# Optimization experiments

Hardware: AMD Instinct MI355X
Metric: run time of the kernel (lower is better)

The kernel has to match this reference:

```python
import jax, jax.numpy as jnp
import numpy as np

B, T = 8, 2048
IN, OUT = 1024, 1024
M, C = 32, 32
MIN_P, MAX_P = 1.0, 1024.0
EPS = 1e-5


def setup_inputs() -> dict:
    key = jax.random.key(0)
    ks = jax.random.split(key, 4)
    x = jax.random.normal(ks[0], (B, T, IN), dtype=jnp.float32)
    # pre: Linear(IN, 2*M + 2*OUT); mix: Linear(2*M*C, OUT)
    pre_w = jax.random.normal(ks[1], (IN, 2 * M + 2 * OUT), dtype=jnp.float32) / np.sqrt(IN)
    pre_b = jnp.zeros((2 * M + 2 * OUT,), jnp.float32)
    mix_w = jax.random.normal(ks[2], (2 * M * C, OUT), dtype=jnp.float32) / np.sqrt(2 * M * C)
    mix_b = jnp.zeros((OUT,), jnp.float32)
    # FFA decay/oscillation params (paper init): gamma_{m,c} = exp(-|a_m| + i b_c)
    a = jnp.linspace(1e-6, 0.5, M, dtype=jnp.float32)
    b = 2.0 * jnp.pi / jnp.linspace(MIN_P, MAX_P, C, dtype=jnp.float32)
    return dict(x=x, pre_w=pre_w, pre_b=pre_b, mix_w=mix_w, mix_b=mix_b, a=a, b=b)


def _ffa(u, a, b):
    """Complex-decay linear recurrence: s_t = gamma * s_{t-1} + u_t (s_0 = 0).

    u: [B,T,M] real input (broadcast over context dim C).
    Returns all states: [B,T,M,C] complex64.
    """
    log_gamma = (-jnp.abs(a))[:, None] + 1j * b[None, :]  # [M,C]
    gamma = jnp.exp(log_gamma).astype(jnp.complex64)
    Tn = u.shape[1]
    h = jnp.broadcast_to(u[..., None].astype(jnp.complex64), u.shape + (C,))  # [B,T,M,C]
    h = jnp.moveaxis(h, 1, 0)  # [T,B,M,C]
    p = jnp.broadcast_to(gamma, (Tn, 1, M, C))  # [T,1,M,C] time-invariant decay

    def combine(e1, e2):
        p1, h1 = e1
        p2, h2 = e2
        return (p1 * p2, h1 * p2 + h2)

    _, hs = jax.lax.associative_scan(combine, (p, h), axis=0)
    return jnp.moveaxis(hs, 0, 1)  # [B,T,M,C]


def reference(x, pre_w, pre_b, mix_w, mix_b, a, b):
    Bx, Tx, _ = x.shape
    pre = x @ pre_w + pre_b  # [B,T,2M+2OUT]
    y, thru, gate = jnp.split(pre, [M, M + OUT], axis=-1)
    gate = jax.nn.sigmoid(gate)
    in_gate, out_gate = gate[..., :M], gate[..., M:]
    s = _ffa(y * in_gate, a, b)  # [B,T,M,C] complex64
    # torch.view_as_real -> [...,M,C,2] then flatten -> interleaved (re,im)
    zr = jnp.stack([s.real, s.imag], axis=-1).reshape(Bx, Tx, 2 * M * C)
    z = zr @ mix_w + mix_b  # [B,T,OUT]
    # LayerNorm (no affine)
    z = (z - z.mean(-1, keepdims=True)) / jnp.sqrt(z.var(-1, keepdims=True) + EPS)
    out = z * out_gate + thru * (1.0 - out_gate)
    return out, s
```

## Files before the change

kernel.cpp:

```cpp
#include <hip/hip_runtime.h>
#include <stdint.h>

typedef __attribute__((ext_vector_type(2))) __bf16 bf16x2;
typedef __attribute__((ext_vector_type(4))) __bf16 bf16x4;
typedef __attribute__((ext_vector_type(8))) __bf16 bf16x8;
typedef __attribute__((ext_vector_type(4))) float f32x4;

#define DEV __device__ __forceinline__

DEV void g2lds16(const void* g, void* l) {
  __builtin_amdgcn_global_load_lds(
      (const __attribute__((address_space(1))) void*)g,
      (__attribute__((address_space(3))) void*)l, 16, 0, 0);
}

DEV void barrier_ws() {
  __builtin_amdgcn_sched_barrier(0);
  asm volatile("" ::: "memory");
  __builtin_amdgcn_s_barrier();
  asm volatile("" ::: "memory");
  __builtin_amdgcn_sched_barrier(0);
}

__global__ __launch_bounds__(256) void cvt_f32_bf16(const float* __restrict__ s,
                                                    __bf16* __restrict__ d, int n) {
  int i = (blockIdx.x * 256 + threadIdx.x) * 4;
  if (i >= n) return;
  float4 v = *reinterpret_cast<const float4*>(s + i);
  bf16x4 o;
  o[0] = (__bf16)v.x; o[1] = (__bf16)v.y; o[2] = (__bf16)v.z; o[3] = (__bf16)v.w;
  *reinterpret_cast<bf16x4*>(d + i) = o;
}

__global__ __launch_bounds__(256) void transpose_to_bf16(const float* __restrict__ src,
                                                         __bf16* __restrict__ dst,
                                                         int K, int N, int Npad) {
  __shared__ float tile[32][33];
  int n0 = blockIdx.x * 32, k0 = blockIdx.y * 32;
  int tx = threadIdx.x & 31, ty = threadIdx.x >> 5;
#pragma unroll
  for (int j = 0; j < 4; ++j) {
    int k = k0 + ty + j * 8;
    int n = n0 + tx;
    float v = 0.f;
    if (n < N) v = src[(long)k * N + n];
    tile[ty + j * 8][tx] = v;
  }
  __syncthreads();
#pragma unroll
  for (int j = 0; j < 4; ++j) {
    int n = n0 + ty + j * 8;
    int k = k0 + tx;
    if (n < Npad) dst[(long)n * K + k] = (__bf16)tile[tx][ty + j * 8];
  }
}

#define STAGE_A(d, kh, kc)                                           \
  { g2lds16(A + aoffg0 + (kc), &As[d][(kh)*8192 + q0 * 8]);          \
    g2lds16(A + aoffg1 + (kc), &As[d][(kh)*8192 + q1 * 8]); }
#define STAGE_B(d, kh, kc)                                           \
  { g2lds16(Wt + boffg0 + (kc), &Bs[d][(kh)*8192 + q0 * 8]);         \
    g2lds16(Wt + boffg1 + (kc), &Bs[d][(kh)*8192 + q1 * 8]); }

#define PHASE(d, MQ, KH, READB, STAGE_STMT, TAILWAIT)                         \
  {                                                                           \
    bf16x8 af[4];                                                             \
    _Pragma("unroll") for (int i = 0; i < 4; ++i)                             \
        af[i] = *reinterpret_cast<const bf16x8*>(                             \
            &As[d][(KH)*8192 + aoffl[(MQ)*4 + i]]);                           \
    if (READB) {                                                              \
      _Pragma("unroll") for (int n = 0; n < 4; ++n)                           \
          bw[n] = *reinterpret_cast<const bf16x8*>(                           \
              &Bs[d][(KH)*8192 + boffl[n]]);                                  \
    }                                                                         \
    STAGE_STMT;                                                               \
    barrier_ws();                                                             \
    __builtin_amdgcn_s_setprio(1);                                            \
    _Pragma("unroll") for (int i = 0; i < 4; ++i)                             \
      _Pragma("unroll") for (int n = 0; n < 4; ++n)                           \
          acc[(MQ)*4 + i][n] = __builtin_amdgcn_mfma_f32_16x16x32_bf16(       \
              af[i], bw[n], acc[(MQ)*4 + i][n], 0, 0, 0);                     \
    __builtin_amdgcn_s_setprio(0);                                            \
    TAILWAIT;                                                                 \
    barrier_ws();                                                             \
  }

template <bool OUT_BF16>
__global__ __launch_bounds__(512, 2) void gemm_8p(const __bf16* __restrict__ A,
                                                  const __bf16* __restrict__ Wt,
                                                  const float* __restrict__ bias,
                                                  void* __restrict__ Cout,
                                                  int K, int Nreal, int ldc,
                                                  int gx) {
  __shared__ __bf16 As[2][16384];
  __shared__ __bf16 Bs[2][16384];
  const int tid = threadIdx.x;
  const int lane = tid & 63, wid = tid >> 6;
  const int wr = wid >> 2, wc = wid & 3;

  const int nwg = gridDim.x;
  const int orig = blockIdx.x;
  const int wg = ((orig & 7) * (nwg >> 3)) + (orig >> 3);
  const int tm = (wg / gx) * 256, tn = (wg % gx) * 256;

  f32x4 acc[8][4] = {};
  bf16x8 bw[4];

  const int q0 = tid, q1 = tid + 512;
  const int row0 = ((q0 >> 3) << 1) | ((q0 >> 2) & 1);
  const int c0e = (((q0 & 3) - (q0 >> 3)) & 3) * 8;
  const int row1 = ((q1 >> 3) << 1) | ((q1 >> 2) & 1);
  const int c1e = (((q1 & 3) - (q1 >> 3)) & 3) * 8;
  const long aoffg0 = (long)(tm + row0) * K + c0e;
  const long aoffg1 = (long)(tm + row1) * K + c1e;
  const long boffg0 = (long)(tn + row0) * K + c0e;
  const long boffg1 = (long)(tn + row1) * K + c1e;

  const int l15 = lane & 15, cl = lane >> 4;
  int aoffl[8], boffl[4];
#pragma unroll
  for (int mf = 0; mf < 8; ++mf) {
    int row = wr * 128 + (mf >> 2) * 64 + (mf & 3) * 16 + l15;
    aoffl[mf] = (row >> 1) * 64 + (((row & 1) << 2) | ((cl + (row >> 1)) & 3)) * 8;
  }
#pragma unroll
  for (int nf = 0; nf < 4; ++nf) {
    int row = wc * 64 + nf * 16 + l15;
    boffl[nf] = (row >> 1) * 64 + (((row & 1) << 2) | ((cl + (row >> 1)) & 3)) * 8;
  }

  STAGE_A(0, 0, 0);
  STAGE_B(0, 0, 0);
  STAGE_A(0, 1, 32);
  STAGE_B(0, 1, 32);
  asm volatile("s_waitcnt vmcnt(4)" ::: "memory");
  barrier_ws();

  const int nt = K >> 6;
  for (int T = 0; T < nt - 1; ++T) {
    const int d = T & 1, e = d ^ 1;
    const int kc = (T + 1) << 6;
    PHASE(d, 0, 0, 1, STAGE_A(e, 0, kc), ((void)0));
    PHASE(d, 1, 0, 0, STAGE_B(e, 0, kc),
          asm volatile("s_waitcnt vmcnt(4)" ::: "memory"));
    PHASE(d, 0, 1, 1, STAGE_A(e, 1, kc + 32), ((void)0));
    PHASE(d, 1, 1, 0, STAGE_B(e, 1, kc + 32),
          asm volatile("s_waitcnt vmcnt(4)" ::: "memory"));
  }
  {
    const int d = (nt - 1) & 1;
    PHASE(d, 0, 0, 1, ((void)0), ((void)0));
    PHASE(d, 1, 0, 0, ((void)0),
          asm volatile("s_waitcnt vmcnt(0)" ::: "memory"));
    PHASE(d, 0, 1, 1, ((void)0), ((void)0));
    PHASE(d, 1, 1, 0, ((void)0), ((void)0));
  }

#pragma unroll
  for (int mf = 0; mf < 8; ++mf) {
    const int rg = tm + wr * 128 + (mf >> 2) * 64 + (mf & 3) * 16 + (lane >> 4) * 4;
#pragma unroll
    for (int nf = 0; nf < 4; ++nf) {
      int col = tn + wc * 64 + nf * 16 + l15;
      if (col < Nreal) {
        float bv = bias[col];
#pragma unroll
        for (int r = 0; r < 4; ++r) {
          long row = rg + r;
          float v = acc[mf][nf][r] + bv;
          if (OUT_BF16) ((__bf16*)Cout)[row * (long)ldc + col] = (__bf16)v;
          else          ((float*)Cout)[row * (long)ldc + col] = v;
        }
      }
    }
  }
}

__global__ __launch_bounds__(256) void u_kernel(const __bf16* __restrict__ pre,
                                                float* __restrict__ u) {
  int i = blockIdx.x * 8 + (threadIdx.x >> 5);
  int m = threadIdx.x & 31;
  const __bf16* pr = pre + (long)i * 2112;
  float y = (float)pr[m];
  float g = (float)pr[1056 + m];
  float sg = 1.f / (1.f + expf(-g));
  int b = i >> 11, t = i & 2047;
  u[(long)((b * 32) + m) * 2048 + t] = y * sg;
}

__global__ __launch_bounds__(64) void scan_kernel(const float* __restrict__ u,
                                                  const float* __restrict__ a,
                                                  const float* __restrict__ bfr,
                                                  __bf16* __restrict__ s_bf,
                                                  float* __restrict__ s_re) {
  int blk = blockIdx.x;
  int b = blk >> 4, mp = blk & 15;
  int lane = threadIdx.x;
  int mh = lane >> 5, c = lane & 31;
  int m = mp * 2 + mh;
  const float* ub = u + (long)(b * 32 + m) * 2048;
  float decay = expf(-fabsf(a[m]));
  float gr = decay * cosf(bfr[c]);
  float gi = decay * sinf(bfr[c]);
  float sr = 0.f, si = 0.f;
  long base = (long)b * 2048 * 1024 + m * 32 + c;
  for (int t = 0; t < 2048; ++t) {
    float uv = ub[t];
    float nr = fmaf(gr, sr, fmaf(-gi, si, uv));
    float ni_ = fmaf(gr, si, gi * sr);
    sr = nr; si = ni_;
    long ci = base + (long)t * 1024;
    bf16x2 zv; zv[0] = (__bf16)sr; zv[1] = (__bf16)si;
    *reinterpret_cast<bf16x2*>(s_bf + 2 * ci) = zv;
    s_re[ci] = sr;
  }
}

__global__ __launch_bounds__(256) void ln_gate_kernel(float* __restrict__ z,
                                                      const __bf16* __restrict__ pre) {
  __shared__ float rs[4], rss[4];
  long row = blockIdx.x;
  float* zp = z + row * 1024;
  int tid = threadIdx.x;
  float4 v = *reinterpret_cast<const float4*>(zp + tid * 4);
  float s = v.x + v.y + v.z + v.w;
  float ss = v.x * v.x + v.y * v.y + v.z * v.z + v.w * v.w;
#pragma unroll
  for (int o = 32; o > 0; o >>= 1) {
    s += __shfl_down(s, o, 64);
    ss += __shfl_down(ss, o, 64);
  }
  if ((tid & 63) == 0) { rs[tid >> 6] = s; rss[tid >> 6] = ss; }
  __syncthreads();
  s = rs[0] + rs[1] + rs[2] + rs[3];
  ss = rss[0] + rss[1] + rss[2] + rss[3];
  float mean = s * (1.f / 1024.f);
  float var = ss * (1.f / 1024.f) - mean * mean;
  float rstd = rsqrtf(var + 1e-5f);
  const __bf16* pr = pre + row * 2112;
  bf16x4 th = *reinterpret_cast<const bf16x4*>(pr + 32 + tid * 4);
  bf16x4 og = *reinterpret_cast<const bf16x4*>(pr + 1088 + tid * 4);
  float4 o; float g;
  g = 1.f / (1.f + expf(-(float)og[0])); o.x = (v.x - mean) * rstd * g + (float)th[0] * (1.f - g);
  g = 1.f / (1.f + expf(-(float)og[1])); o.y = (v.y - mean) * rstd * g + (float)th[1] * (1.f - g);
  g = 1.f / (1.f + expf(-(float)og[2])); o.z = (v.z - mean) * rstd * g + (float)th[2] * (1.f - g);
  g = 1.f / (1.f + expf(-(float)og[3])); o.w = (v.w - mean) * rstd * g + (float)th[3] * (1.f - g);
  *reinterpret_cast<float4*>(zp + tid * 4) = o;
}

extern "C" void kernel_launch(void* const* d_in, const int* in_sizes, int n_in,
                              void* d_out, int out_size, void* d_ws, size_t ws_size,
                              hipStream_t stream) {
  const float* x = (const float*)d_in[0];
  const float* pre_w = (const float*)d_in[1];
  const float* pre_b = (const float*)d_in[2];
  const float* mix_w = (const float*)d_in[3];
  const float* mix_b = (const float*)d_in[4];
  const float* a = (const float*)d_in[5];
  const float* bfr = (const float*)d_in[6];

  char* ws = (char*)d_ws;
  __bf16* buf0  = (__bf16*)(ws + 0);
  __bf16* wtbuf = (__bf16*)(ws + 67108864);
  __bf16* pre   = (__bf16*)(ws + 71827456);
  float*  u     = (float*)(ws + 141033472);
  const size_t WS_NEEDED = 143130624ull;
  if (ws_size < WS_NEEDED) return;

  __bf16* x_bf = buf0;
  __bf16* s_bf = buf0;

  float* out0 = (float*)d_out;
  float* s_re = out0 + 16777216;

  cvt_f32_bf16<<<16384, 256, 0, stream>>>(x, x_bf, 16777216);
  transpose_to_bf16<<<dim3(72, 32), 256, 0, stream>>>(pre_w, wtbuf, 1024, 2112, 2304);
  gemm_8p<true><<<576, 512, 0, stream>>>(x_bf, wtbuf, pre_b, pre, 1024, 2112, 2112, 9);
  u_kernel<<<2048, 256, 0, stream>>>(pre, u);
  transpose_to_bf16<<<dim3(32, 64), 256, 0, stream>>>(mix_w, wtbuf, 2048, 1024, 1024);
  scan_kernel<<<128, 64, 0, stream>>>(u, a, bfr, s_bf, s_re);
  gemm_8p<false><<<256, 512, 0, stream>>>(s_bf, wtbuf, mix_b, out0, 2048, 1024, 1024, 4);
  ln_gate_kernel<<<16384, 256, 0, stream>>>(out0, pre);
}
```

Before: 339.9 us.

## Restructure GEMM main loop with register double-buffered fragments and fewer barriers

The bf16 GEMM main loop drops its eight-phase macro, which put two barriers around every 4x4 MFMA block (eight per K-tile), in favour of two barriers per K-tile. A fragments are double-buffered in registers (afc/afn), so the LDS reads for the next MFMA block are issued while the current block computes. The global-to-LDS staging loads are interleaved between MFMA blocks. The sched_barrier fences are removed, which leaves instruction ordering to the compiler; this saves barrier stalls but costs extra VGPRs and may be scheduled less predictably.

```diff
diff --git a/kernel.cpp b/kernel.cpp
--- a/kernel.cpp
+++ b/kernel.cpp
@@ -14,13 +14,13 @@
       (__attribute__((address_space(3))) void*)l, 16, 0, 0);
 }
 
-DEV void barrier_ws() {
-  __builtin_amdgcn_sched_barrier(0);
+DEV void bar() {
   asm volatile("" ::: "memory");
   __builtin_amdgcn_s_barrier();
   asm volatile("" ::: "memory");
-  __builtin_amdgcn_sched_barrier(0);
-}
+}
+DEV void vm4() { asm volatile("s_waitcnt vmcnt(4)" ::: "memory"); }
+DEV void vm0() { asm volatile("s_waitcnt vmcnt(0)" ::: "memory"); }
 
 __global__ __launch_bounds__(256) void cvt_f32_bf16(const float* __restrict__ s,
                                                     __bf16* __restrict__ d, int n) {
@@ -55,35 +55,29 @@
   }
 }
 
-#define STAGE_A(d, kh, kc)                                           \
-  { g2lds16(A + aoffg0 + (kc), &As[d][(kh)*8192 + q0 * 8]);          \
-    g2lds16(A + aoffg1 + (kc), &As[d][(kh)*8192 + q1 * 8]); }
-#define STAGE_B(d, kh, kc)                                           \
-  { g2lds16(Wt + boffg0 + (kc), &Bs[d][(kh)*8192 + q0 * 8]);         \
-    g2lds16(Wt + boffg1 + (kc), &Bs[d][(kh)*8192 + q1 * 8]); }
-
-#define PHASE(d, MQ, KH, READB, STAGE_STMT, TAILWAIT)                         \
-  {                                                                           \
-    bf16x8 af[4];                                                             \
-    _Pragma("unroll") for (int i = 0; i < 4; ++i)                             \
-        af[i] = *reinterpret_cast<const bf16x8*>(                             \
-            &As[d][(KH)*8192 + aoffl[(MQ)*4 + i]]);                           \
-    if (READB) {                                                              \
-      _Pragma("unroll") for (int n = 0; n < 4; ++n)                           \
-          bw[n] = *reinterpret_cast<const bf16x8*>(                           \
-              &Bs[d][(KH)*8192 + boffl[n]]);                                  \
-    }                                                                         \
-    STAGE_STMT;                                                               \
-    barrier_ws();                                                             \
-    __builtin_amdgcn_s_setprio(1);                                            \
-    _Pragma("unroll") for (int i = 0; i < 4; ++i)                             \
-      _Pragma("unroll") for (int n = 0; n < 4; ++n)                           \
-          acc[(MQ)*4 + i][n] = __builtin_amdgcn_mfma_f32_16x16x32_bf16(       \
-              af[i], bw[n], acc[(MQ)*4 + i][n], 0, 0, 0);                     \
-    __builtin_amdgcn_s_setprio(0);                                            \
-    TAILWAIT;                                                                 \
-    barrier_ws();                                                             \
-  }
+#define STAGE_A(e, kh, kc)                                           \
+  { g2lds16(A + aoffg0 + (kc), &As[e][(kh)*8192 + q0 * 8]);          \
+    g2lds16(A + aoffg1 + (kc), &As[e][(kh)*8192 + q1 * 8]); }
+#define STAGE_B(e, kh, kc)                                           \
+  { g2lds16(Wt + boffg0 + (kc), &Bs[e][(kh)*8192 + q0 * 8]);         \
+    g2lds16(Wt + boffg1 + (kc), &Bs[e][(kh)*8192 + q1 * 8]); }
+
+#define READ_A(dst, MQ, KH, D)                                       \
+  _Pragma("unroll") for (int i = 0; i < 4; ++i)                      \
+      dst[i] = *reinterpret_cast<const bf16x8*>(                     \
+          &As[D][(KH)*8192 + aoffl[(MQ)*4 + i]]);
+#define READ_B(dst, KH, D)                                           \
+  _Pragma("unroll") for (int n = 0; n < 4; ++n)                      \
+      dst[n] = *reinterpret_cast<const bf16x8*>(                     \
+          &Bs[D][(KH)*8192 + boffl[n]]);
+
+#define MFMA_BLK(MQ, AF, BW)                                                  \
+  __builtin_amdgcn_s_setprio(1);                                              \
+  _Pragma("unroll") for (int i = 0; i < 4; ++i)                               \
+    _Pragma("unroll") for (int n = 0; n < 4; ++n)                             \
+        acc[(MQ)*4 + i][n] = __builtin_amdgcn_mfma_f32_16x16x32_bf16(         \
+            AF[i], BW[n], acc[(MQ)*4 + i][n], 0, 0, 0);                       \
+  __builtin_amdgcn_s_setprio(0);
 
 template <bool OUT_BF16>
 __global__ __launch_bounds__(512, 2) void gemm_8p(const __bf16* __restrict__ A,
@@ -104,7 +98,7 @@
   const int tm = (wg / gx) * 256, tn = (wg % gx) * 256;
 
   f32x4 acc[8][4] = {};
-  bf16x8 bw[4];
+  bf16x8 afc[4], afn[4], bwc[4];
 
   const int q0 = tid, q1 = tid + 512;
   const int row0 = ((q0 >> 3) << 1) | ((q0 >> 2) & 1);
@@ -133,27 +127,46 @@
   STAGE_B(0, 0, 0);
   STAGE_A(0, 1, 32);
   STAGE_B(0, 1, 32);
-  asm volatile("s_waitcnt vmcnt(4)" ::: "memory");
-  barrier_ws();
+  vm4();
+  bar();
+  READ_A(afc, 0, 0, 0);
+  READ_B(bwc, 0, 0);
 
   const int nt = K >> 6;
   for (int T = 0; T < nt - 1; ++T) {
     const int d = T & 1, e = d ^ 1;
     const int kc = (T + 1) << 6;
-    PHASE(d, 0, 0, 1, STAGE_A(e, 0, kc), ((void)0));
-    PHASE(d, 1, 0, 0, STAGE_B(e, 0, kc),
-          asm volatile("s_waitcnt vmcnt(4)" ::: "memory"));
-    PHASE(d, 0, 1, 1, STAGE_A(e, 1, kc + 32), ((void)0));
-    PHASE(d, 1, 1, 0, STAGE_B(e, 1, kc + 32),
-          asm volatile("s_waitcnt vmcnt(4)" ::: "memory"));
+    STAGE_A(e, 0, kc);
+    READ_A(afn, 1, 0, d);
+    MFMA_BLK(0, afc, bwc);
+    STAGE_B(e, 0, kc);
+    MFMA_BLK(1, afn, bwc);
+    vm4();
+    bar();
+    READ_A(afc, 0, 1, d);
+    READ_B(bwc, 1, d);
+    STAGE_A(e, 1, kc + 32);
+    READ_A(afn, 1, 1, d);
+    MFMA_BLK(0, afc, bwc);
+    STAGE_B(e, 1, kc + 32);
+    MFMA_BLK(1, afn, bwc);
+    vm4();
+    bar();
+    READ_A(afc, 0, 0, e);
+    READ_B(bwc, 0, e);
   }
   {
     const int d = (nt - 1) & 1;
-    PHASE(d, 0, 0, 1, ((void)0), ((void)0));
-    PHASE(d, 1, 0, 0, ((void)0),
-          asm volatile("s_waitcnt vmcnt(0)" ::: "memory"));
-    PHASE(d, 0, 1, 1, ((void)0), ((void)0));
-    PHASE(d, 1, 1, 0, ((void)0), ((void)0));
+    READ_A(afn, 1, 0, d);
+    MFMA_BLK(0, afc, bwc);
+    MFMA_BLK(1, afn, bwc);
+    vm0();
+    bar();
+    READ_A(afc, 0, 1, d);
+    READ_B(bwc, 1, d);
+    READ_A(afn, 1, 1, d);
+    MFMA_BLK(0, afc, bwc);
+    MFMA_BLK(1, afn, bwc);
   }
 
 #pragma unroll
```

New measurement: 325.8 us. 1.04x faster.

## Replace 256x256 double-buffered GEMM with 128x128 triple-buffered pipeline

Applied to the files above, without the earlier changes.

Both GEMMs now use a new kernel with 128x128 output tiles, 256 threads, three LDS stages of K=32, and compile-time K with hand-unrolled stage rotation. This replaces the 512-thread 256x256 kernel that used four sub-phases and two barriers per phase. The goal is more workgroups for better CU occupancy and load balance, less N-padding waste on the 2112-wide first GEMM, and fewer barriers per K step. In exchange, each tile gets less operand reuse per LDS load, which raises global and LDS traffic.

```diff
diff --git a/kernel.cpp b/kernel.cpp
--- a/kernel.cpp
+++ b/kernel.cpp
@@ -13,14 +13,13 @@
       (const __attribute__((address_space(1))) void*)g,
       (__attribute__((address_space(3))) void*)l, 16, 0, 0);
 }
-
-DEV void barrier_ws() {
-  __builtin_amdgcn_sched_barrier(0);
+DEV void bar() {
   asm volatile("" ::: "memory");
   __builtin_amdgcn_s_barrier();
   asm volatile("" ::: "memory");
-  __builtin_amdgcn_sched_barrier(0);
-}
+}
+DEV void vm4() { asm volatile("s_waitcnt vmcnt(4)" ::: "memory"); }
+DEV void vm0() { asm volatile("s_waitcnt vmcnt(0)" ::: "memory"); }
 
 __global__ __launch_bounds__(256) void cvt_f32_bf16(const float* __restrict__ s,
                                                     __bf16* __restrict__ d, int n) {
@@ -55,113 +54,104 @@
   }
 }
 
-#define STAGE_A(d, kh, kc)                                           \
-  { g2lds16(A + aoffg0 + (kc), &As[d][(kh)*8192 + q0 * 8]);          \
-    g2lds16(A + aoffg1 + (kc), &As[d][(kh)*8192 + q1 * 8]); }
-#define STAGE_B(d, kh, kc)                                           \
-  { g2lds16(Wt + boffg0 + (kc), &Bs[d][(kh)*8192 + q0 * 8]);         \
-    g2lds16(Wt + boffg1 + (kc), &Bs[d][(kh)*8192 + q1 * 8]); }
-
-#define PHASE(d, MQ, KH, READB, STAGE_STMT, TAILWAIT)                         \
-  {                                                                           \
-    bf16x8 af[4];                                                             \
-    _Pragma("unroll") for (int i = 0; i < 4; ++i)                             \
-        af[i] = *reinterpret_cast<const bf16x8*>(                             \
-            &As[d][(KH)*8192 + aoffl[(MQ)*4 + i]]);                           \
-    if (READB) {                                                              \
-      _Pragma("unroll") for (int n = 0; n < 4; ++n)                           \
-          bw[n] = *reinterpret_cast<const bf16x8*>(                           \
-              &Bs[d][(KH)*8192 + boffl[n]]);                                  \
-    }                                                                         \
-    STAGE_STMT;                                                               \
-    barrier_ws();                                                             \
-    __builtin_amdgcn_s_setprio(1);                                            \
-    _Pragma("unroll") for (int i = 0; i < 4; ++i)                             \
-      _Pragma("unroll") for (int n = 0; n < 4; ++n)                           \
-          acc[(MQ)*4 + i][n] = __builtin_amdgcn_mfma_f32_16x16x32_bf16(       \
-              af[i], bw[n], acc[(MQ)*4 + i][n], 0, 0, 0);                     \
-    __builtin_amdgcn_s_setprio(0);                                            \
-    TAILWAIT;                                                                 \
-    barrier_ws();                                                             \
-  }
-
-template <bool OUT_BF16>
-__global__ __launch_bounds__(512, 2) void gemm_8p(const __bf16* __restrict__ A,
+#define STAGE3(BUF, KC)                                              \
+  { g2lds16(A + aoffg0 + (KC), &As[BUF][q0 * 8]);                    \
+    g2lds16(A + aoffg1 + (KC), &As[BUF][q1 * 8]);                    \
+    g2lds16(Wt + boffg0 + (KC), &Bs[BUF][q0 * 8]);                   \
+    g2lds16(Wt + boffg1 + (KC), &Bs[BUF][q1 * 8]); }
+
+#define COMPUTE3(CUR)                                                \
+  { bf16x8 af[4], bw[4];                                             \
+    _Pragma("unroll") for (int i = 0; i < 4; ++i)                    \
+        af[i] = *reinterpret_cast<const bf16x8*>(&As[CUR][aoffl[i]]);\
+    _Pragma("unroll") for (int n = 0; n < 4; ++n)                    \
+        bw[n] = *reinterpret_cast<const bf16x8*>(&Bs[CUR][boffl[n]]);\
+    __builtin_amdgcn_s_setprio(1);                                   \
+    _Pragma("unroll") for (int i = 0; i < 4; ++i)                    \
+      _Pragma("unroll") for (int n = 0; n < 4; ++n)                  \
+          acc[i][n] = __builtin_amdgcn_mfma_f32_16x16x32_bf16(       \
+              af[i], bw[n], acc[i][n], 0, 0, 0);                     \
+    __builtin_amdgcn_s_setprio(0); }
+
+#define ITER3(CUR, STG, KC) \
+  STAGE3(STG, KC); COMPUTE3(CUR); vm4(); bar();
+
+template <bool OUT_BF16, int K>
+__global__ __launch_bounds__(256, 3) void gemm_p3(const __bf16* __restrict__ A,
                                                   const __bf16* __restrict__ Wt,
                                                   const float* __restrict__ bias,
                                                   void* __restrict__ Cout,
-                                                  int K, int Nreal, int ldc,
-                                                  int gx) {
-  __shared__ __bf16 As[2][16384];
-  __shared__ __bf16 Bs[2][16384];
+                                                  int Nreal, int ldc, int gx) {
+  __shared__ __bf16 As[3][4096];
+  __shared__ __bf16 Bs[3][4096];
   const int tid = threadIdx.x;
   const int lane = tid & 63, wid = tid >> 6;
-  const int wr = wid >> 2, wc = wid & 3;
 
   const int nwg = gridDim.x;
   const int orig = blockIdx.x;
   const int wg = ((orig & 7) * (nwg >> 3)) + (orig >> 3);
-  const int tm = (wg / gx) * 256, tn = (wg % gx) * 256;
-
-  f32x4 acc[8][4] = {};
-  bf16x8 bw[4];
-
-  const int q0 = tid, q1 = tid + 512;
+  const int tm = (wg / gx) * 128, tn = (wg % gx) * 128;
+
+  f32x4 acc[4][4] = {};
+
+  const int q0 = tid, q1 = tid + 256;
   const int row0 = ((q0 >> 3) << 1) | ((q0 >> 2) & 1);
   const int c0e = (((q0 & 3) - (q0 >> 3)) & 3) * 8;
-  const int row1 = ((q1 >> 3) << 1) | ((q1 >> 2) & 1);
-  const int c1e = (((q1 & 3) - (q1 >> 3)) & 3) * 8;
+  const int row1 = row0 + 64;
   const long aoffg0 = (long)(tm + row0) * K + c0e;
-  const long aoffg1 = (long)(tm + row1) * K + c1e;
+  const long aoffg1 = (long)(tm + row1) * K + c0e;
   const long boffg0 = (long)(tn + row0) * K + c0e;
-  const long boffg1 = (long)(tn + row1) * K + c1e;
+  const long boffg1 = (long)(tn + row1) * K + c0e;
 
   const int l15 = lane & 15, cl = lane >> 4;
-  int aoffl[8], boffl[4];
-#pragma unroll
-  for (int mf = 0; mf < 8; ++mf) {
-    int row = wr * 128 + (mf >> 2) * 64 + (mf & 3) * 16 + l15;
+  int aoffl[4], boffl[4];
+#pragma unroll
+  for (int mf = 0; mf < 4; ++mf) {
+    int row = (wid >> 1) * 64 + mf * 16 + l15;
     aoffl[mf] = (row >> 1) * 64 + (((row & 1) << 2) | ((cl + (row >> 1)) & 3)) * 8;
   }
 #pragma unroll
   for (int nf = 0; nf < 4; ++nf) {
-    int row = wc * 64 + nf * 16 + l15;
+    int row = (wid & 1) * 64 + nf * 16 + l15;
     boffl[nf] = (row >> 1) * 64 + (((row & 1) << 2) | ((cl + (row >> 1)) & 3)) * 8;
   }
 
-  STAGE_A(0, 0, 0);
-  STAGE_B(0, 0, 0);
-  STAGE_A(0, 1, 32);
-  STAGE_B(0, 1, 32);
-  asm volatile("s_waitcnt vmcnt(4)" ::: "memory");
-  barrier_ws();
-
-  const int nt = K >> 6;
-  for (int T = 0; T < nt - 1; ++T) {
-    const int d = T & 1, e = d ^ 1;
-    const int kc = (T + 1) << 6;
-    PHASE(d, 0, 0, 1, STAGE_A(e, 0, kc), ((void)0));
-    PHASE(d, 1, 0, 0, STAGE_B(e, 0, kc),
-          asm volatile("s_waitcnt vmcnt(4)" ::: "memory"));
-    PHASE(d, 0, 1, 1, STAGE_A(e, 1, kc + 32), ((void)0));
-    PHASE(d, 1, 1, 0, STAGE_B(e, 1, kc + 32),
-          asm volatile("s_waitcnt vmcnt(4)" ::: "memory"));
-  }
-  {
-    const int d = (nt - 1) & 1;
-    PHASE(d, 0, 0, 1, ((void)0), ((void)0));
-    PHASE(d, 1, 0, 0, ((void)0),
-          asm volatile("s_waitcnt vmcnt(0)" ::: "memory"));
-    PHASE(d, 0, 1, 1, ((void)0), ((void)0));
-    PHASE(d, 1, 1, 0, ((void)0), ((void)0));
-  }
-
-#pragma unroll
-  for (int mf = 0; mf < 8; ++mf) {
-    const int rg = tm + wr * 128 + (mf >> 2) * 64 + (mf & 3) * 16 + (lane >> 4) * 4;
+  constexpr int nt = K >> 5;
+  STAGE3(0, 0);
+  STAGE3(1, 32);
+  vm4();
+  bar();
+
+  if constexpr (K == 1024) {
+#pragma unroll 1
+    for (int i = 0; i < 10; ++i) {
+      const int kc = (3 * i + 2) << 5;
+      ITER3(0, 2, kc);
+      ITER3(1, 0, kc + 32);
+      ITER3(2, 1, kc + 64);
+    }
+    COMPUTE3(0); vm0(); bar();
+    COMPUTE3(1);
+  } else {
+    ITER3(0, 2, 64);
+    ITER3(1, 0, 96);
+#pragma unroll 1
+    for (int i = 0; i < 20; ++i) {
+      const int kc = (3 * i + 4) << 5;
+      ITER3(2, 1, kc);
+      ITER3(0, 2, kc + 32);
+      ITER3(1, 0, kc + 64);
+    }
+    COMPUTE3(2); vm0(); bar();
+    COMPUTE3(0);
+  }
+
+#pragma unroll
+  for (int mf = 0; mf < 4; ++mf) {
+    const int rg = tm + (wid >> 1) * 64 + mf * 16 + (lane >> 4) * 4;
 #pragma unroll
     for (int nf = 0; nf < 4; ++nf) {
-      int col = tn + wc * 64 + nf * 16 + l15;
+      int col = tn + (wid & 1) * 64 + nf * 16 + l15;
       if (col < Nreal) {
         float bv = bias[col];
 #pragma unroll
@@ -274,11 +264,13 @@
   float* s_re = out0 + 16777216;
 
   cvt_f32_bf16<<<16384, 256, 0, stream>>>(x, x_bf, 16777216);
-  transpose_to_bf16<<<dim3(72, 32), 256, 0, stream>>>(pre_w, wtbuf, 1024, 2112, 2304);
-  gemm_8p<true><<<576, 512, 0, stream>>>(x_bf, wtbuf, pre_b, pre, 1024, 2112, 2112, 9);
+  transpose_to_bf16<<<dim3(68, 32), 256, 0, stream>>>(pre_w, wtbuf, 1024, 2112, 2176);
+  gemm_p3<true, 1024><<<2176, 256, 0, stream>>>(x_bf, wtbuf, pre_b, pre,
+                                                2112, 2112, 17);
   u_kernel<<<2048, 256, 0, stream>>>(pre, u);
   transpose_to_bf16<<<dim3(32, 64), 256, 0, stream>>>(mix_w, wtbuf, 2048, 1024, 1024);
   scan_kernel<<<128, 64, 0, stream>>>(u, a, bfr, s_bf, s_re);
-  gemm_8p<false><<<256, 512, 0, stream>>>(s_bf, wtbuf, mix_b, out0, 2048, 1024, 1024, 4);
+  gemm_p3<false, 2048><<<1024, 256, 0, stream>>>(s_bf, wtbuf, mix_b, out0,
+                                                 1024, 1024, 8);
   ln_gate_kernel<<<16384, 256, 0, stream>>>(out0, pre);
 }
```

Result: no change. 337.9 us (-0.6%).
